# Kernel tuning notes

Hardware: AMD Instinct MI355X
Metric: run time of the kernel (lower is better)

The kernel has to match this reference:

```python
import jax, jax.numpy as jnp
import numpy as np

B, N, F, H1, H2, NC = 1024, 64, 1024, 256, 128, 128
ALPHA = 0.2   # LeakyReLU slope
BN_EPS = 1e-5


def setup_inputs() -> dict:
    key = jax.random.key(0)
    ks = jax.random.split(key, 20)
    d = {}
    d["x"] = jax.random.normal(ks[0], (B, 1, F), dtype=jnp.float32)
    d["neighbor"] = jax.random.normal(ks[1], (B, N, 1, F), dtype=jnp.float32)
    # GraphAttn layer 1 params
    d["W1"] = jax.random.normal(ks[2], (H1, F), dtype=jnp.float32) / np.sqrt(F)
    d["b1"] = jnp.zeros((H1,), dtype=jnp.float32)
    d["a11"] = jax.random.normal(ks[3], (H1,), dtype=jnp.float32) / np.sqrt(H1)
    d["a12"] = jax.random.normal(ks[4], (H1,), dtype=jnp.float32) / np.sqrt(H1)
    d["g1"] = jnp.ones((), dtype=jnp.float32)   # BatchNorm1d(1) weight (scalar)
    d["be1"] = jnp.zeros((), dtype=jnp.float32)  # BatchNorm1d(1) bias
    # GraphAttn layer 2 params
    d["W2"] = jax.random.normal(ks[5], (H2, H1), dtype=jnp.float32) / np.sqrt(H1)
    d["b2"] = jnp.zeros((H2,), dtype=jnp.float32)
    d["a21"] = jax.random.normal(ks[6], (H2,), dtype=jnp.float32) / np.sqrt(H2)
    d["a22"] = jax.random.normal(ks[7], (H2,), dtype=jnp.float32) / np.sqrt(H2)
    d["g2"] = jnp.ones((), dtype=jnp.float32)
    d["be2"] = jnp.zeros((), dtype=jnp.float32)
    # final classifier
    d["Wl"] = jax.random.normal(ks[8], (NC, H2), dtype=jnp.float32) / np.sqrt(H2)
    d["bl"] = jnp.zeros((NC,), dtype=jnp.float32)
    return d


def _l2norm_c(t):
    # torch nf.normalize default: p=2, dim=1 -> here the singleton channel axis (-2)
    n = jnp.sqrt(jnp.sum(t * t, axis=-2, keepdims=True))
    return t / jnp.maximum(n, 1e-12)


def _gat_layer(x, nb, W, b, a_self, a_nb):
    # x: [B,1,Fin], nb: [B,N,1,Fin]
    xh = jnp.einsum('bcf,hf->bch', x, W) + b        # [B,1,H]
    nbh = jnp.einsum('bncf,hf->bnch', nb, W) + b    # [B,N,1,H]
    # att1(x[i]) + att2(neighbor[i]) -> scores over N (C==1 squeezed)
    s = (jnp.einsum('bch,h->bc', xh, a_self)[:, None, :]
         + jnp.einsum('bnch,h->bnc', nbh, a_nb))[..., 0]   # [B,N]
    A = jax.nn.softmax(jax.nn.leaky_relu(s, ALPHA), axis=1)  # softmax over neighbors
    out = jnp.einsum('bn,bnch->bch', A, nbh)        # [B,1,H]
    return out, nbh


def _bn_relu(t, g, b, axes):
    # BatchNorm1d(1) in training mode: stats over all non-channel dims of the tensor
    m = jnp.mean(t, axis=axes, keepdims=True)
    v = jnp.mean(jnp.square(t - m), axis=axes, keepdims=True)
    return jax.nn.relu(g * (t - m) * jax.lax.rsqrt(v + BN_EPS) + b)


def reference(x, neighbor, W1, b1, a11, a12, g1, be1,
              W2, b2, a21, a22, g2, be2, Wl, bl):
    x = _l2norm_c(x)
    nb = _l2norm_c(neighbor)
    x, nb = _gat_layer(x, nb, W1, b1, a11, a12)
    # acvt1 applied to x [B,1,H1] (stats over B,H) and to each neighbor tensor
    # [N,1,H1] separately (per-sample stats -> axes (1,3) of [B,N,1,H1])
    x = _bn_relu(x, g1, be1, axes=(0, 2))
    nb = _bn_relu(nb, g1, be1, axes=(1, 3))
    x, nb = _gat_layer(x, nb, W2, b2, a21, a22)
    x = _bn_relu(x, g2, be2, axes=(0, 2))
    # Flatten -> Dropout(p=0) -> Linear
    logits = jnp.einsum('bh,ch->bc', x.reshape(x.shape[0], -1), Wl) + bl
    return logits
```

## Files before the change

### kernel.cpp

```cpp
#include <hip/hip_runtime.h>
#include <hip/hip_bf16.h>
#include <stdint.h>

#define B_    1024
#define N_    64
#define F_    1024
#define H1_   256
#define H2_   128
#define NC_   128
#define ALPHA 0.2f
#define BN_EPS 1e-5f

typedef __attribute__((ext_vector_type(4))) float  f32x4;
typedef __attribute__((ext_vector_type(8))) __bf16 bf16x8;
typedef __attribute__((ext_vector_type(4))) __bf16 bf16x4;

__device__ inline float sign_ref(float v) {
    float s = copysignf(1.0f, v);
    return (fabsf(v) >= 1e-12f) ? s : v * 1e12f;
}

__device__ __forceinline__ void gload_lds16(const void* g, void* l) {
    auto gp = reinterpret_cast<const __attribute__((address_space(1))) void*>(
        reinterpret_cast<uintptr_t>(g));
    auto lp = reinterpret_cast<__attribute__((address_space(3))) void*>(
        reinterpret_cast<uintptr_t>(l));
    __builtin_amdgcn_global_load_lds(gp, lp, 16, 0, 0);
}

__device__ inline float blk_reduce(float v, float* buf) {
    #pragma unroll
    for (int o = 32; o > 0; o >>= 1) v += __shfl_xor(v, o, 64);
    __syncthreads();
    const int wave = threadIdx.x >> 6, lane = threadIdx.x & 63;
    if (lane == 0) buf[wave] = v;
    __syncthreads();
    float r = 0.f;
    if (threadIdx.x == 0) {
        const int nw = blockDim.x >> 6;
        for (int i = 0; i < nw; ++i) r += buf[i];
    }
    return r;
}

__global__ __launch_bounds__(256) void k_prep(
    const float* __restrict__ W1, const float* __restrict__ W2,
    const float* __restrict__ b1, const float* __restrict__ a11,
    const float* __restrict__ a12, const float* __restrict__ b2,
    const float* __restrict__ a21, const float* __restrict__ a22,
    __bf16* __restrict__ W1b, __bf16* __restrict__ W2b,
    float* __restrict__ w1a, float* __restrict__ w2a,
    float* __restrict__ w2a22, float* __restrict__ cscal)
{
    __shared__ float rbuf[8];
    const int blk = blockIdx.x, tid = threadIdx.x;
    if (blk < 256) {
        const int i0 = blk * 1024 + tid * 4;
        float4 v = *(const float4*)(W1 + i0);
        bf16x4 p = { (__bf16)v.x, (__bf16)v.y, (__bf16)v.z, (__bf16)v.w };
        *(bf16x4*)(W1b + i0) = p;
    } else if (blk < 288) {
        const int i0 = (blk - 256) * 1024 + tid * 4;
        float4 v = *(const float4*)(W2 + i0);
        bf16x4 p = { (__bf16)v.x, (__bf16)v.y, (__bf16)v.z, (__bf16)v.w };
        *(bf16x4*)(W2b + i0) = p;
    } else if (blk < 292) {
        const int f = (blk - 288) * 256 + tid;
        float s1 = 0.f;
        #pragma unroll 8
        for (int h = 0; h < H1_; ++h) s1 += W1[h * F_ + f] * a11[h];
        w1a[f] = s1;
    } else if (blk == 292) {
        float s1 = 0.f, s2 = 0.f;
        #pragma unroll 8
        for (int h = 0; h < H2_; ++h) {
            const float w = W2[h * H1_ + tid];
            s1 += w * a21[h]; s2 += w * a22[h];
        }
        w2a[tid] = s1; w2a22[tid] = s2;
    } else {
        float v1 = b1[tid] * a11[tid];
        float v2 = (tid < H2_) ? b2[tid] * a21[tid] : 0.f;
        float v3 = (tid < H2_) ? b2[tid] * a22[tid] : 0.f;
        float r1 = blk_reduce(v1, rbuf);
        float r2 = blk_reduce(v2, rbuf);
        float r3 = blk_reduce(v3, rbuf);
        if (tid == 0) { cscal[0] = r1; cscal[1] = r2; cscal[2] = r3; }
    }
}

__global__ __launch_bounds__(256, 2) void k_gemm1(
    const float* __restrict__ A, const __bf16* __restrict__ Bw,
    const float* __restrict__ bias, __bf16* __restrict__ C,
    const float* __restrict__ x, const float* __restrict__ w1a,
    const float* __restrict__ a12, const float* __restrict__ w2a22,
    const float* __restrict__ cscal, const float* __restrict__ g1p,
    const float* __restrict__ be1p,
    float* __restrict__ out1, float* __restrict__ alpha1,
    float* __restrict__ beta1, float* __restrict__ psum1,
    float* __restrict__ psq1, float* __restrict__ spart)
{
    constexpr int BM = 64, BK = 64, K = F_;
    constexpr int LDA = BK + 8;
    __shared__ __attribute__((aligned(16))) char smem[BM * LDA * 2 + 256 * BK * 2];
    __bf16* As = (__bf16*)smem;
    __bf16* Bs = (__bf16*)(smem + BM * LDA * 2);
    __bf16* Cs = Bs;
    __shared__ float a12s[H1_];
    __shared__ float w2a22s[H1_];
    __shared__ float sv[N_];
    __shared__ float rbuf[8];
    __shared__ float fscal[4];

    const int tid = threadIdx.x;
    const int wave = tid >> 6, lane = tid & 63;
    const int rowin = lane & 15, kq = lane >> 4;
    const size_t b = blockIdx.x;

    {
        const float* xb = x + b * F_;
        float p0 = 0.f;
        #pragma unroll
        for (int i = 0; i < 4; ++i)
            p0 += sign_ref(xb[tid + i * 256]) * w1a[tid + i * 256];
        a12s[tid] = a12[tid]; w2a22s[tid] = w2a22[tid];
        float r0 = blk_reduce(p0, rbuf);
        if (tid == 0) fscal[0] = r0 + cscal[0];
    }

    f32x4 acc[4][4] = {};

    const int cqA = tid & 15, r0A = tid >> 4;
    const float* Abase = A + b * (size_t)BM * K + cqA * 4;

    for (int k0 = 0; k0 < K; k0 += BK) {
        #pragma unroll
        for (int it = 0; it < 8; ++it) {
            const int s = it * 256 + tid;
            const int r = s >> 3;
            const int c8 = (s & 7) ^ (r & 7);
            gload_lds16(Bw + (size_t)r * K + k0 + c8 * 8, Bs + s * 8);
        }
        #pragma unroll
        for (int rr = 0; rr < 4; ++rr) {
            const int r = r0A + rr * 16;
            float4 v = *(const float4*)(Abase + (size_t)r * K + k0);
            bf16x4 p = { (__bf16)sign_ref(v.x), (__bf16)sign_ref(v.y),
                         (__bf16)sign_ref(v.z), (__bf16)sign_ref(v.w) };
            *(bf16x4*)&As[r * LDA + cqA * 4] = p;
        }
        __syncthreads();
        #pragma unroll
        for (int ks = 0; ks < 2; ++ks) {
            bf16x8 af[4], bv[4];
            #pragma unroll
            for (int mi = 0; mi < 4; ++mi)
                af[mi] = *(const bf16x8*)&As[(mi * 16 + rowin) * LDA + ks * 32 + kq * 8];
            #pragma unroll
            for (int ni = 0; ni < 4; ++ni) {
                const int r = wave * 64 + ni * 16 + rowin;
                const int c = (ks * 4 + kq) ^ (r & 7);
                bv[ni] = *(const bf16x8*)&Bs[(r * 8 + c) * 8];
            }
            #pragma unroll
            for (int mi = 0; mi < 4; ++mi)
                #pragma unroll
                for (int ni = 0; ni < 4; ++ni)
                    acc[mi][ni] = __builtin_amdgcn_mfma_f32_16x16x32_bf16(
                        af[mi], bv[ni], acc[mi][ni], 0, 0, 0);
        }
        __syncthreads();
    }

    const int cr0 = (lane >> 4) * 4, cc = lane & 15;
    #pragma unroll
    for (int ni = 0; ni < 4; ++ni) {
        const int col = wave * 64 + ni * 16 + cc;
        const float bs = bias[col];
        #pragma unroll
        for (int mi = 0; mi < 4; ++mi)
            #pragma unroll
            for (int i = 0; i < 4; ++i)
                Cs[(mi * 16 + cr0 + i) * 256 + col] = (__bf16)(acc[mi][ni][i] + bs);
    }
    __syncthreads();
    #pragma unroll
    for (int it = 0; it < 8; ++it) {
        const int s = it * 256 + tid;
        *(bf16x8*)(C + (b * 64 + (s >> 5)) * 256 + (s & 31) * 8) =
            *(const bf16x8*)&Cs[s * 8];
    }
    {
        const int n = tid >> 2, q = tid & 3;
        float p = 0.f;
        for (int i = 0; i < 64; ++i) {
            const int h = q * 64 + ((i + tid) & 63);
            p += (float)Cs[n * 256 + h] * a12s[h];
        }
        p += __shfl_xor(p, 1); p += __shfl_xor(p, 2);
        if (q == 0) { float s = fscal[0] + p; sv[n] = s > 0.f ? s : ALPHA * s; }
    }
    __syncthreads();
    if (tid < 64) {
        float s = sv[tid], m = s;
        #pragma unroll
        for (int o = 1; o < 64; o <<= 1) m = fmaxf(m, __shfl_xor(m, o));
        float e = __expf(s - m), t = e;
        #pragma unroll
        for (int o = 1; o < 64; o <<= 1) t += __shfl_xor(t, o);
        sv[tid] = e / t;
    }
    __syncthreads();
    float o1 = 0.f, ss = 0.f, sq = 0.f;
    for (int n2 = 0; n2 < N_; ++n2) {
        const float v = (float)Cs[n2 * 256 + tid];
        o1 += sv[n2] * v; ss += v; sq += v * v;
    }
    out1[b * H1_ + tid] = o1;
    {
        const float rs = blk_reduce(ss, rbuf);
        const float rq = blk_reduce(sq, rbuf);
        if (tid == 0) {
            const float inv = 1.f / (float)(N_ * H1_);
            const float mean = rs * inv, var = rq * inv - mean * mean;
            const float a = (*g1p) * rsqrtf(var + BN_EPS);
            const float bb = (*be1p) - a * mean;
            alpha1[b] = a; beta1[b] = bb;
            fscal[2] = a; fscal[3] = bb;
        }
        const float rsx = blk_reduce(o1, rbuf);
        const float rqx = blk_reduce(o1 * o1, rbuf);
        if (tid == 0) { psum1[b] = rsx; psq1[b] = rqx; }
    }
    __syncthreads();
    {
        const float al_ = fscal[2], be_ = fscal[3];
        const int n = tid >> 2, q = tid & 3;
        float p = 0.f;
        for (int i = 0; i < 64; ++i) {
            const int h = q * 64 + ((i + tid) & 63);
            const float v = (float)Cs[n * 256 + h];
            p += fmaxf(fmaf(al_, v, be_), 0.f) * w2a22s[h];
        }
        p += __shfl_xor(p, 1); p += __shfl_xor(p, 2);
        if (q == 0) spart[b * N_ + n] = p;
    }
}

__global__ __launch_bounds__(256) void k_back(
    const __bf16* __restrict__ nbh1, const float* __restrict__ out1,
    const float* __restrict__ alpha1, const float* __restrict__ beta1,
    const float* __restrict__ psum1, const float* __restrict__ psq1,
    const float* __restrict__ g1p, const float* __restrict__ be1p,
    const float* __restrict__ w2a, const float* __restrict__ spart,
    const float* __restrict__ cscal, const __bf16* __restrict__ W2b,
    const float* __restrict__ b2,
    float* __restrict__ out2, float* __restrict__ psum2,
    float* __restrict__ psq2)
{
    __shared__ __attribute__((aligned(16))) __bf16 tile[N_ * H1_];
    __shared__ float w2as[H1_];
    __shared__ float sv[N_];
    __shared__ float g2s[H1_ + 8];
    __shared__ float hpart[H2_];
    __shared__ float rbuf[8];
    __shared__ float scal[3];

    const int b = blockIdx.x, tid = threadIdx.x;

    const __bf16* src = nbh1 + (size_t)b * N_ * H1_;
    #pragma unroll
    for (int it = 0; it < 8; ++it)
        gload_lds16(src + (it * 256 + tid) * 8, tile + (it * 256 + tid) * 8);
    w2as[tid] = w2a[tid];
    const float o1 = out1[(size_t)b * H1_ + tid];
    const float al = alpha1[b], be = beta1[b];

    {
        float s = 0.f, q = 0.f;
        for (int i = tid; i < B_; i += 256) { s += psum1[i]; q += psq1[i]; }
        const float gs = blk_reduce(s, rbuf);
        const float gq = blk_reduce(q, rbuf);
        if (tid == 0) {
            const float n = (float)(B_ * H1_);
            const float mean = gs / n, var = gq / n - mean * mean;
            const float a = (*g1p) * rsqrtf(var + BN_EPS);
            scal[0] = a; scal[1] = (*be1p) - a * mean;
        }
    }
    __syncthreads();

    {
        const float x2 = fmaxf(fmaf(scal[0], o1, scal[1]), 0.f);
        const float r = blk_reduce(x2 * w2as[tid], rbuf);
        if (tid == 0) scal[2] = r + cscal[1] + cscal[2];
    }
    __syncthreads();

    if (tid < 64) {
        float s = scal[2] + spart[(size_t)b * N_ + tid];
        s = s > 0.f ? s : ALPHA * s;
        float m = s;
        #pragma unroll
        for (int o = 1; o < 64; o <<= 1) m = fmaxf(m, __shfl_xor(m, o));
        float e = __expf(s - m), t = e;
        #pragma unroll
        for (int o = 1; o < 64; o <<= 1) t += __shfl_xor(t, o);
        sv[tid] = e / t;
    }
    __syncthreads();

    {
        float g = 0.f;
        for (int n2 = 0; n2 < N_; ++n2) {
            const float v = (float)tile[n2 * H1_ + tid];
            g += sv[n2] * fmaxf(fmaf(al, v, be), 0.f);
        }
        g2s[tid + (tid >> 5)] = g;
    }
    __syncthreads();

    #pragma unroll 4
    for (int j = 0; j < 16; ++j) {
        const int idx = j * 256 + tid;
        const int h = idx >> 5, k8 = idx & 31;
        const bf16x8 w = ((const bf16x8*)W2b)[idx];
        float p = 0.f;
        #pragma unroll
        for (int i = 0; i < 8; ++i) {
            const int k = k8 * 8 + i;
            p += (float)w[i] * g2s[k + (k >> 5)];
        }
        p += __shfl_xor(p, 1); p += __shfl_xor(p, 2); p += __shfl_xor(p, 4);
        p += __shfl_xor(p, 8); p += __shfl_xor(p, 16);
        if ((tid & 31) == 0) hpart[h] = p;
    }
    __syncthreads();
    {
        float o2 = 0.f;
        if (tid < H2_) o2 = hpart[tid] + b2[tid];
        const float rs2 = blk_reduce(o2, rbuf);
        const float rq2 = blk_reduce(o2 * o2, rbuf);
        if (tid < H2_) out2[(size_t)b * H2_ + tid] = o2;
        if (tid == 0) { psum2[b] = rs2; psq2[b] = rq2; }
    }
}

__global__ __launch_bounds__(128) void k_fin(
    const float* __restrict__ out2, const float* __restrict__ psum2,
    const float* __restrict__ psq2, const float* __restrict__ g2p,
    const float* __restrict__ be2p, const float* __restrict__ Wl,
    const float* __restrict__ bl, float* __restrict__ logits)
{
    __shared__ float xr[H2_];
    __shared__ float Ws[NC_][H2_ + 1];
    __shared__ float axbx[2];
    __shared__ float rbuf[8];
    const int b = blockIdx.x, tid = threadIdx.x;
    {
        float s = 0.f, q = 0.f;
        for (int i = tid; i < B_; i += 128) { s += psum2[i]; q += psq2[i]; }
        const float gs = blk_reduce(s, rbuf);
        const float gq = blk_reduce(q, rbuf);
        if (tid == 0) {
            const float n = (float)(B_ * H2_);
            const float mean = gs / n, var = gq / n - mean * mean;
            const float a = (*g2p) * rsqrtf(var + BN_EPS);
            axbx[0] = a; axbx[1] = (*be2p) - a * mean;
        }
    }
    for (int i = tid; i < NC_ * H2_ / 4; i += 128) {
        float4 v = ((const float4*)Wl)[i];
        const int r = i >> 5, c = (i & 31) * 4;
        Ws[r][c] = v.x; Ws[r][c + 1] = v.y; Ws[r][c + 2] = v.z; Ws[r][c + 3] = v.w;
    }
    __syncthreads();
    xr[tid] = fmaxf(fmaf(axbx[0], out2[(size_t)b * H2_ + tid], axbx[1]), 0.f);
    __syncthreads();
    float acc = bl[tid];
    #pragma unroll 4
    for (int h = 0; h < H2_; ++h) acc += xr[h] * Ws[tid][h];
    logits[(size_t)b * NC_ + tid] = acc;
}

extern "C" void kernel_launch(void* const* d_in, const int* in_sizes, int n_in,
                              void* d_out, int out_size, void* d_ws, size_t ws_size,
                              hipStream_t stream)
{
    const float* x   = (const float*)d_in[0];
    const float* nb  = (const float*)d_in[1];
    const float* W1  = (const float*)d_in[2];
    const float* b1  = (const float*)d_in[3];
    const float* a11 = (const float*)d_in[4];
    const float* a12 = (const float*)d_in[5];
    const float* g1  = (const float*)d_in[6];
    const float* be1 = (const float*)d_in[7];
    const float* W2  = (const float*)d_in[8];
    const float* b2  = (const float*)d_in[9];
    const float* a21 = (const float*)d_in[10];
    const float* a22 = (const float*)d_in[11];
    const float* g2  = (const float*)d_in[12];
    const float* be2 = (const float*)d_in[13];
    const float* Wl  = (const float*)d_in[14];
    const float* bl  = (const float*)d_in[15];
    float* logits = (float*)d_out;

    size_t off = 0;
    auto alc = [&](size_t bytes) {
        void* p = (char*)d_ws + off;
        off = (off + bytes + 255) & ~(size_t)255;
        return p;
    };
    __bf16* W1b   = (__bf16*)alc((size_t)H1_ * F_ * 2);
    __bf16* W2b   = (__bf16*)alc((size_t)H2_ * H1_ * 2);
    float* w1a    = (float*)alc(F_ * 4);
    float* w2a    = (float*)alc(H1_ * 4);
    float* w2a22  = (float*)alc(H1_ * 4);
    float* cscal  = (float*)alc(3 * 4);
    float* alpha1 = (float*)alc(B_ * 4);
    float* beta1  = (float*)alc(B_ * 4);
    float* psum1  = (float*)alc(B_ * 4);
    float* psq1   = (float*)alc(B_ * 4);
    float* psum2  = (float*)alc(B_ * 4);
    float* psq2   = (float*)alc(B_ * 4);
    float* spart  = (float*)alc((size_t)B_ * N_ * 4);
    float* out1   = (float*)alc((size_t)B_ * H1_ * 4);
    float* out2   = (float*)alc((size_t)B_ * H2_ * 4);
    __bf16* nbh1  = (__bf16*)alc((size_t)B_ * N_ * H1_ * 2);

    k_prep<<<294, 256, 0, stream>>>(W1, W2, b1, a11, a12, b2, a21, a22,
                                    W1b, W2b, w1a, w2a, w2a22, cscal);
    k_gemm1<<<B_, 256, 0, stream>>>(
        nb, W1b, b1, nbh1, x, w1a, a12, w2a22, cscal, g1, be1,
        out1, alpha1, beta1, psum1, psq1, spart);
    k_back<<<B_, 256, 0, stream>>>(nbh1, out1, alpha1, beta1, psum1, psq1,
                                   g1, be1, w2a, spart, cscal, W2b, b2,
                                   out2, psum2, psq2);
    k_fin<<<B_, 128, 0, stream>>>(out2, psum2, psq2, g2, be2, Wl, bl, logits);
}
```

Baseline: 467.6 us.

## Pre-swizzle W1 into MFMA fragment order and double-buffer A tiles in gemm1

The W1 prep step now writes bf16 weights directly in per-lane MFMA fragment order, so each wave loads its B operands straight from global memory (L2-resident) instead of staging them through LDS. This frees LDS for a double-buffered A tile: the next 64-wide slice of A is loaded into registers while the current one runs through the MFMAs. With less LDS per block, launch bounds go up to 3 blocks per CU. The cost is more global/L2 traffic for B per block and more register pressure from the prefetched A values.

```diff
diff --git a/kernel.cpp b/kernel.cpp
--- a/kernel.cpp
+++ b/kernel.cpp
@@ -48,17 +48,19 @@
     const float* __restrict__ b1, const float* __restrict__ a11,
     const float* __restrict__ a12, const float* __restrict__ b2,
     const float* __restrict__ a21, const float* __restrict__ a22,
-    __bf16* __restrict__ W1b, __bf16* __restrict__ W2b,
+    __bf16* __restrict__ W1f, __bf16* __restrict__ W2b,
     float* __restrict__ w1a, float* __restrict__ w2a,
     float* __restrict__ w2a22, float* __restrict__ cscal)
 {
     __shared__ float rbuf[8];
     const int blk = blockIdx.x, tid = threadIdx.x;
     if (blk < 256) {
-        const int i0 = blk * 1024 + tid * 4;
-        float4 v = *(const float4*)(W1 + i0);
+        const int h = blk, k0 = tid * 4;
+        float4 v = *(const float4*)(W1 + h * F_ + k0);
         bf16x4 p = { (__bf16)v.x, (__bf16)v.y, (__bf16)v.z, (__bf16)v.w };
-        *(bf16x4*)(W1b + i0) = p;
+        const int kc = k0 >> 5, kq = (k0 >> 3) & 3, j = k0 & 7;
+        const int rbk = h >> 4, rowin = h & 15;
+        *(bf16x4*)(W1f + (size_t)((kc * 16 + rbk) * 64 + kq * 16 + rowin) * 8 + j) = p;
     } else if (blk < 288) {
         const int i0 = (blk - 256) * 1024 + tid * 4;
         float4 v = *(const float4*)(W2 + i0);
@@ -89,7 +91,7 @@
     }
 }
 
-__global__ __launch_bounds__(256, 2) void k_gemm1(
+__global__ __launch_bounds__(256, 3) void k_gemm1(
     const float* __restrict__ A, const __bf16* __restrict__ Bw,
     const float* __restrict__ bias, __bf16* __restrict__ C,
     const float* __restrict__ x, const float* __restrict__ w1a,
@@ -100,12 +102,12 @@
     float* __restrict__ beta1, float* __restrict__ psum1,
     float* __restrict__ psq1, float* __restrict__ spart)
 {
-    constexpr int BM = 64, BK = 64, K = F_;
-    constexpr int LDA = BK + 8;
-    __shared__ __attribute__((aligned(16))) char smem[BM * LDA * 2 + 256 * BK * 2];
-    __bf16* As = (__bf16*)smem;
-    __bf16* Bs = (__bf16*)(smem + BM * LDA * 2);
-    __bf16* Cs = Bs;
+    constexpr int K = F_;
+    constexpr int LDA = 72;
+    __shared__ __attribute__((aligned(16))) char smem[64 * 256 * 2];
+    __bf16* As0 = (__bf16*)smem;
+    __bf16* As1 = As0 + 64 * LDA;
+    __bf16* Cs  = (__bf16*)smem;
     __shared__ float a12s[H1_];
     __shared__ float w2a22s[H1_];
     __shared__ float sv[N_];
@@ -131,37 +133,18 @@
     f32x4 acc[4][4] = {};
 
     const int cqA = tid & 15, r0A = tid >> 4;
-    const float* Abase = A + b * (size_t)BM * K + cqA * 4;
-
-    for (int k0 = 0; k0 < K; k0 += BK) {
-        #pragma unroll
-        for (int it = 0; it < 8; ++it) {
-            const int s = it * 256 + tid;
-            const int r = s >> 3;
-            const int c8 = (s & 7) ^ (r & 7);
-            gload_lds16(Bw + (size_t)r * K + k0 + c8 * 8, Bs + s * 8);
-        }
-        #pragma unroll
-        for (int rr = 0; rr < 4; ++rr) {
-            const int r = r0A + rr * 16;
-            float4 v = *(const float4*)(Abase + (size_t)r * K + k0);
-            bf16x4 p = { (__bf16)sign_ref(v.x), (__bf16)sign_ref(v.y),
-                         (__bf16)sign_ref(v.z), (__bf16)sign_ref(v.w) };
-            *(bf16x4*)&As[r * LDA + cqA * 4] = p;
-        }
-        __syncthreads();
+    const float* Abase = A + b * (size_t)64 * K + cqA * 4;
+
+    auto mfma_phase = [&](const __bf16* buf, int kc0) {
         #pragma unroll
         for (int ks = 0; ks < 2; ++ks) {
             bf16x8 af[4], bv[4];
             #pragma unroll
             for (int mi = 0; mi < 4; ++mi)
-                af[mi] = *(const bf16x8*)&As[(mi * 16 + rowin) * LDA + ks * 32 + kq * 8];
+                af[mi] = *(const bf16x8*)&buf[(mi * 16 + rowin) * LDA + ks * 32 + kq * 8];
             #pragma unroll
-            for (int ni = 0; ni < 4; ++ni) {
-                const int r = wave * 64 + ni * 16 + rowin;
-                const int c = (ks * 4 + kq) ^ (r & 7);
-                bv[ni] = *(const bf16x8*)&Bs[(r * 8 + c) * 8];
-            }
+            for (int ni = 0; ni < 4; ++ni)
+                bv[ni] = ((const bf16x8*)Bw)[((kc0 + ks) * 16 + wave * 4 + ni) * 64 + lane];
             #pragma unroll
             for (int mi = 0; mi < 4; ++mi)
                 #pragma unroll
@@ -169,8 +152,44 @@
                     acc[mi][ni] = __builtin_amdgcn_mfma_f32_16x16x32_bf16(
                         af[mi], bv[ni], acc[mi][ni], 0, 0, 0);
         }
-        __syncthreads();
-    }
+    };
+    auto stage = [&](__bf16* buf, const float4* av) {
+        #pragma unroll
+        for (int rr = 0; rr < 4; ++rr) {
+            const float4 v = av[rr];
+            bf16x4 p = { (__bf16)sign_ref(v.x), (__bf16)sign_ref(v.y),
+                         (__bf16)sign_ref(v.z), (__bf16)sign_ref(v.w) };
+            *(bf16x4*)&buf[(r0A + rr * 16) * LDA + cqA * 4] = p;
+        }
+    };
+
+    float4 avA[4], avB[4];
+    #pragma unroll
+    for (int rr = 0; rr < 4; ++rr)
+        avA[rr] = *(const float4*)(Abase + (size_t)(r0A + rr * 16) * K);
+
+    for (int kk = 0; kk < 8; ++kk) {
+        const int k0 = kk * 128;
+        #pragma unroll
+        for (int rr = 0; rr < 4; ++rr)
+            avB[rr] = *(const float4*)(Abase + (size_t)(r0A + rr * 16) * K + k0 + 64);
+        stage(As0, avA);
+        asm volatile("s_waitcnt lgkmcnt(0)" ::: "memory");
+        __builtin_amdgcn_s_barrier();
+        __builtin_amdgcn_sched_barrier(0);
+        mfma_phase(As0, kk * 4);
+        if (kk < 7) {
+            #pragma unroll
+            for (int rr = 0; rr < 4; ++rr)
+                avA[rr] = *(const float4*)(Abase + (size_t)(r0A + rr * 16) * K + k0 + 128);
+        }
+        stage(As1, avB);
+        asm volatile("s_waitcnt lgkmcnt(0)" ::: "memory");
+        __builtin_amdgcn_s_barrier();
+        __builtin_amdgcn_sched_barrier(0);
+        mfma_phase(As1, kk * 4 + 2);
+    }
+    __syncthreads();
 
     const int cr0 = (lane >> 4) * 4, cc = lane & 15;
     #pragma unroll
@@ -411,7 +430,7 @@
         off = (off + bytes + 255) & ~(size_t)255;
         return p;
     };
-    __bf16* W1b   = (__bf16*)alc((size_t)H1_ * F_ * 2);
+    __bf16* W1f   = (__bf16*)alc((size_t)H1_ * F_ * 2);
     __bf16* W2b   = (__bf16*)alc((size_t)H2_ * H1_ * 2);
     float* w1a    = (float*)alc(F_ * 4);
     float* w2a    = (float*)alc(H1_ * 4);
@@ -429,9 +448,9 @@
     __bf16* nbh1  = (__bf16*)alc((size_t)B_ * N_ * H1_ * 2);
 
     k_prep<<<294, 256, 0, stream>>>(W1, W2, b1, a11, a12, b2, a21, a22,
-                                    W1b, W2b, w1a, w2a, w2a22, cscal);
+                                    W1f, W2b, w1a, w2a, w2a22, cscal);
     k_gemm1<<<B_, 256, 0, stream>>>(
-        nb, W1b, b1, nbh1, x, w1a, a12, w2a22, cscal, g1, be1,
+        nb, W1f, b1, nbh1, x, w1a, a12, w2a22, cscal, g1, be1,
         out1, alpha1, beta1, psum1, psq1, spart);
     k_back<<<B_, 256, 0, stream>>>(nbh1, out1, alpha1, beta1, psum1, psq1,
                                    g1, be1, w2a, spart, cscal, W2b, b2,
```

Result: slower. 493.4 us (+5.5%).
